# Optimization experiments

Hardware: AMD Instinct MI355X
Metric: run time of the kernel (lower is better)

The kernel has to match this reference:

```python
import jax, jax.numpy as jnp
import numpy as np

NPOINT, RADIUS, NSAMPLE = 1024, 0.4, 32
BN_EPS = 1e-5


def fps(xyz, npoint):
    # xyz: [B, N, 3]. Deterministic start at index 0 (torch uses randint).
    B, N, _ = xyz.shape

    def step(carry, _):
        distance, farthest = carry  # [B,N], [B]
        centroid = jnp.take_along_axis(xyz, farthest[:, None, None], axis=1)  # [B,1,3]
        dist = jnp.sum((xyz - centroid) ** 2, -1)  # [B,N]
        distance = jnp.minimum(distance, dist)
        new_far = jnp.argmax(distance, axis=-1).astype(jnp.int32)
        return (distance, new_far), farthest

    init = (jnp.full((B, N), 1e10, xyz.dtype), jnp.zeros((B,), jnp.int32))
    _, cents = jax.lax.scan(step, init, None, length=npoint)  # [npoint, B]
    return cents.T  # [B, npoint]


def square_distance(src, dst):
    # src [B,S,3], dst [B,N,3] -> [B,S,N]
    d = -2.0 * jnp.einsum('bsc,bnc->bsn', src, dst)
    d = d + jnp.sum(src ** 2, -1)[:, :, None] + jnp.sum(dst ** 2, -1)[:, None, :]
    return jnp.clip(d, 1e-12, None)


def query_ball_point(radius, nsample, xyz, new_xyz):
    B, N, _ = xyz.shape
    S = new_xyz.shape[1]
    sqr = square_distance(new_xyz, xyz)  # [B,S,N]
    gi = jnp.where(sqr > radius ** 2, N, jnp.arange(N, dtype=jnp.int32)[None, None, :])
    gi = jnp.sort(gi, axis=-1)[:, :, :nsample]  # [B,S,K]
    first = gi[:, :, :1]
    return jnp.where(gi == N, first, gi)


def gather_points(points, idx):
    # points [B,N,C], idx [B,S,K] -> [B,S,K,C]
    B, S, K = idx.shape
    C = points.shape[-1]
    flat = jnp.take_along_axis(points, idx.reshape(B, S * K)[:, :, None], axis=1)
    return flat.reshape(B, S, K, C)


def setup_inputs() -> dict:
    key = jax.random.key(0)
    ks = jax.random.split(key, 10)
    B, N, D = 8, 4096, 64
    inp = {
        'xyz': jax.random.normal(ks[0], (B, 3, N), jnp.float32),
        'points': jax.random.normal(ks[1], (B, D, N), jnp.float32),
    }
    chans = [67, 64, 64, 128]
    for i in range(3):
        cin, cout = chans[i], chans[i + 1]
        inp[f'W{i}'] = jax.random.normal(ks[2 + i], (cout, cin), jnp.float32) * (1.0 / np.sqrt(cin))
        inp[f'b{i}'] = jnp.zeros((cout,), jnp.float32)
        inp[f'g{i}'] = jnp.ones((cout,), jnp.float32)
        inp[f'bt{i}'] = jnp.zeros((cout,), jnp.float32)
    return inp


def _forward(xyz, points, Ws, bs, gs, bts):
    xyz_t = jnp.transpose(xyz, (0, 2, 1))      # [B,N,3]
    pts_t = jnp.transpose(points, (0, 2, 1))   # [B,N,D]
    B, N, _ = xyz_t.shape

    fps_idx = fps(xyz_t, NPOINT)                              # [B,S]
    new_xyz = jnp.take_along_axis(xyz_t, fps_idx[:, :, None], axis=1)  # [B,S,3]
    idx = query_ball_point(RADIUS, NSAMPLE, xyz_t, new_xyz)   # [B,S,K]

    grouped_xyz = gather_points(xyz_t, idx)                   # [B,S,K,3]
    grouped_xyz_norm = grouped_xyz - new_xyz[:, :, None, :]
    grouped_pts = gather_points(pts_t, idx)                   # [B,S,K,D]
    new_points = jnp.concatenate([grouped_xyz_norm, grouped_pts], -1)  # [B,S,K,3+D]

    x = jnp.transpose(new_points, (0, 3, 2, 1))  # [B,C,K,S]
    for W, b, g, bt in zip(Ws, bs, gs, bts):
        x = jnp.einsum('oc,bcks->boks', W, x) + b[None, :, None, None]
        mean = jnp.mean(x, axis=(0, 2, 3), keepdims=True)
        var = jnp.var(x, axis=(0, 2, 3), keepdims=True)
        x = (x - mean) * jax.lax.rsqrt(var + BN_EPS)
        x = x * g[None, :, None, None] + bt[None, :, None, None]
        x = jax.nn.relu(x)
    out = jnp.max(x, axis=2)                      # [B,C_out,S]
    return jnp.transpose(new_xyz, (0, 2, 1)), out


def reference(xyz, points, W0, b0, g0, bt0, W1, b1, g1, bt1, W2, b2, g2, bt2):
    return _forward(xyz, points, (W0, W1, W2), (b0, b1, b2), (g0, g1, g2), (bt0, bt1, bt2))
```

## Files before the change

### kernel.cpp

```cpp
#include <hip/hip_runtime.h>
#include <cstddef>
#include <cstdint>

#define NB 8
#define NPTS 4096
#define NS 1024
#define NK 32
#define ND 64

typedef __attribute__((ext_vector_type(8))) short bf16x8;
typedef __attribute__((ext_vector_type(4))) float f32x4;

__device__ __forceinline__ short f2bf(float f) {
  unsigned u = __float_as_uint(f);
  u += 0x7FFF + ((u >> 16) & 1);
  return (short)(u >> 16);
}

#define DPP_IMAX(v, ctrl)                                                     \
  {                                                                           \
    int _o = __builtin_amdgcn_update_dpp(v, v, ctrl, 0xf, 0xf, false);        \
    v = (_o > v) ? _o : v;                                                    \
  }

#define DPP_U64MAX(hi, lo, ctrl)                                              \
  {                                                                           \
    unsigned _nh = (unsigned)__builtin_amdgcn_update_dpp((int)(hi), (int)(hi),\
                                                         ctrl, 0xf, 0xf, false);\
    unsigned _nl = (unsigned)__builtin_amdgcn_update_dpp((int)(lo), (int)(lo),\
                                                         ctrl, 0xf, 0xf, false);\
    bool _gt = (_nh > (hi)) || (_nh == (hi) && _nl > (lo));                   \
    hi = _gt ? _nh : (hi);                                                    \
    lo = _gt ? _nl : (lo);                                                    \
  }

#define DPP_FADD(v, ctrl)                                                     \
  {                                                                           \
    int _t = __builtin_amdgcn_update_dpp(__float_as_int(v), __float_as_int(v),\
                                         ctrl, 0xf, 0xf, false);              \
    v = v + __int_as_float(_t);                                               \
  }

#define DPP_RED16(v, OP)                                                      \
  {                                                                           \
    int _i;                                                                   \
    _i = __builtin_amdgcn_update_dpp(__float_as_int(v), __float_as_int(v), 0x111, 0xf, 0xf, false); \
    v = OP(v, __int_as_float(_i));                                            \
    _i = __builtin_amdgcn_update_dpp(__float_as_int(v), __float_as_int(v), 0x112, 0xf, 0xf, false); \
    v = OP(v, __int_as_float(_i));                                            \
    _i = __builtin_amdgcn_update_dpp(__float_as_int(v), __float_as_int(v), 0x114, 0xf, 0xf, false); \
    v = OP(v, __int_as_float(_i));                                            \
    _i = __builtin_amdgcn_update_dpp(__float_as_int(v), __float_as_int(v), 0x118, 0xf, 0xf, false); \
    v = OP(v, __int_as_float(_i));                                            \
  }

__device__ __forceinline__ float fadd_op(float a, float b) { return a + b; }

__global__ __launch_bounds__(512) void fps_pgemm_kernel(
    const float* __restrict__ xyz, float* __restrict__ out_newxyz,
    float* __restrict__ ws_newxyz, const float* __restrict__ points,
    const float* __restrict__ W0, const float* __restrict__ b0g,
    float* __restrict__ P1) {
  __shared__ __align__(16) char smem[53376];
  const int t = threadIdx.x;

  if (blockIdx.x < 8) {
    float* sXYZ = (float*)smem;
    unsigned long long(*sRed)[8] =
        (unsigned long long(*)[8])(smem + 49152);
    int* sWidx = (int*)(smem + 49280);
    const int b = blockIdx.x;
    const int wave = t >> 6;
    const int lane = t & 63;
    const float* xb = xyz + (size_t)b * 3 * NPTS;

    for (int i = t; i < NPTS; i += 512) {
      sXYZ[i * 3 + 0] = xb[i];
      sXYZ[i * 3 + 1] = xb[NPTS + i];
      sXYZ[i * 3 + 2] = xb[2 * NPTS + i];
    }
    if (t == 0) sWidx[0] = 0;

    float px[8], py[8], pz[8], dist[8];
    {
      float4 a0 = ((const float4*)xb)[2 * t];
      float4 a1 = ((const float4*)xb)[2 * t + 1];
      float4 b0v = ((const float4*)(xb + NPTS))[2 * t];
      float4 b1v = ((const float4*)(xb + NPTS))[2 * t + 1];
      float4 c0 = ((const float4*)(xb + 2 * NPTS))[2 * t];
      float4 c1 = ((const float4*)(xb + 2 * NPTS))[2 * t + 1];
      px[0] = a0.x; px[1] = a0.y; px[2] = a0.z; px[3] = a0.w;
      px[4] = a1.x; px[5] = a1.y; px[6] = a1.z; px[7] = a1.w;
      py[0] = b0v.x; py[1] = b0v.y; py[2] = b0v.z; py[3] = b0v.w;
      py[4] = b1v.x; py[5] = b1v.y; py[6] = b1v.z; py[7] = b1v.w;
      pz[0] = c0.x; pz[1] = c0.y; pz[2] = c0.z; pz[3] = c0.w;
      pz[4] = c1.x; pz[5] = c1.y; pz[6] = c1.z; pz[7] = c1.w;
    }
#pragma unroll
    for (int j = 0; j < 8; ++j) dist[j] = 1e10f;

    float cx = xb[0], cy = xb[NPTS], cz = xb[2 * NPTS];

    for (int s = 0; s < NS; ++s) {
#pragma unroll
      for (int j = 0; j < 8; ++j) {
        float dx = __fadd_rn(px[j], -cx);
        float dy = __fadd_rn(py[j], -cy);
        float dz = __fadd_rn(pz[j], -cz);
        float d = __fadd_rn(__fadd_rn(__fmul_rn(dx, dx), __fmul_rn(dy, dy)),
                            __fmul_rn(dz, dz));
        dist[j] = fminf(dist[j], d);
      }
      float m = fmaxf(fmaxf(fmaxf(dist[0], dist[1]), fmaxf(dist[2], dist[3])),
                      fmaxf(fmaxf(dist[4], dist[5]), fmaxf(dist[6], dist[7])));
      int v = __float_as_int(m);
      DPP_IMAX(v, 0x111)
      DPP_IMAX(v, 0x112)
      DPP_IMAX(v, 0x114)
      DPP_IMAX(v, 0x118)
      DPP_IMAX(v, 0x142)
      DPP_IMAX(v, 0x143)
      const int wm_i = __builtin_amdgcn_readlane(v, 63);
      const float wm = __int_as_float(wm_i);
      unsigned long long claim = __ballot(m == wm);
      int firstlane = __ffsll(claim) - 1;
      if (lane == firstlane) {
        int j = 7;
#pragma unroll
        for (int jj = 6; jj >= 0; --jj)
          if (dist[jj] == wm) j = jj;
        unsigned widx = (unsigned)(t * 8 + j);
        sRed[s & 1][wave] = ((unsigned long long)(unsigned)wm_i << 32) |
                            (unsigned long long)(0xFFFFFFFFu - widx);
      }
      __syncthreads();
      unsigned long long k = sRed[s & 1][lane & 7];
      unsigned h2 = (unsigned)(k >> 32), l2 = (unsigned)k;
      DPP_U64MAX(h2, l2, 0x111)
      DPP_U64MAX(h2, l2, 0x112)
      DPP_U64MAX(h2, l2, 0x114)
      const unsigned gl = (unsigned)__builtin_amdgcn_readlane((int)l2, 7);
      const int widx = (int)(0xFFFFFFFFu - gl);
      cx = sXYZ[widx * 3 + 0];
      cy = sXYZ[widx * 3 + 1];
      cz = sXYZ[widx * 3 + 2];
      if (t == 0 && s < NS - 1) sWidx[s + 1] = widx;
    }
    __syncthreads();
    for (int s2 = t; s2 < NS; s2 += 512) {
      int w = sWidx[s2];
      float x = sXYZ[w * 3 + 0], y = sXYZ[w * 3 + 1], z = sXYZ[w * 3 + 2];
      out_newxyz[b * 3 * NS + s2] = x;
      out_newxyz[b * 3 * NS + NS + s2] = y;
      out_newxyz[b * 3 * NS + 2 * NS + s2] = z;
      ws_newxyz[((b << 10) + s2) * 3 + 0] = x;
      ws_newxyz[((b << 10) + s2) * 3 + 1] = y;
      ws_newxyz[((b << 10) + s2) * 3 + 2] = z;
    }
  } else {
    float* sP = (float*)smem;
    float* sW = (float*)(smem + 16384);
    float* sB = (float*)(smem + 33792);
    const int blk = blockIdx.x - 8;
    const int bb = blk >> 6;
    const int n0 = (blk & 63) * 64;
    const float* pb = points + (size_t)bb * ND * NPTS;
    for (int f = t; f < 4096; f += 512) {
      int c = f >> 6, n = f & 63;
      sP[f] = pb[c * NPTS + n0 + n];
    }
    for (int f = t; f < 4096; f += 512) {
      int c = f >> 6, o = f & 63;
      sW[c * 68 + o] = W0[o * 67 + 3 + c];
    }
    if (t < 64) sB[t] = b0g[t];
    __syncthreads();
    if (t < 256) {
      const int nl = (t & 15) * 4;
      const int ol = (t >> 4) * 4;
      float acc[4][4];
#pragma unroll
      for (int i = 0; i < 4; ++i)
#pragma unroll
        for (int j = 0; j < 4; ++j) acc[i][j] = 0.f;
#pragma unroll 4
      for (int c = 0; c < 64; ++c) {
        float4 xv = *(const float4*)(sP + c * 64 + nl);
        float4 wv = *(const float4*)(sW + c * 68 + ol);
        float xa[4] = {xv.x, xv.y, xv.z, xv.w};
        float wa[4] = {wv.x, wv.y, wv.z, wv.w};
#pragma unroll
        for (int i = 0; i < 4; ++i)
#pragma unroll
          for (int j = 0; j < 4; ++j) acc[i][j] += xa[i] * wa[j];
      }
#pragma unroll
      for (int i = 0; i < 4; ++i) {
        float4 v = make_float4(acc[i][0] + sB[ol + 0], acc[i][1] + sB[ol + 1],
                               acc[i][2] + sB[ol + 2], acc[i][3] + sB[ol + 3]);
        *(float4*)(P1 + ((size_t)(bb << 12) + n0 + nl + i) * 64 + ol) = v;
      }
    }
  }
}

__global__ __launch_bounds__(256) void query_gstats_kernel(
    const float* __restrict__ xyz, const float* __restrict__ ws_newxyz,
    const float* __restrict__ P1, const float* __restrict__ W0,
    int* __restrict__ idx_ws, float* __restrict__ partials) {
  const int w = threadIdx.x >> 6;
  const int lane = threadIdx.x & 63;
  const int p = blockIdx.x * 4 + w;
  const int b = p >> 10;
  __shared__ int sIdx[4][32];
  __shared__ float sWS[4][64];
  __shared__ float sWQ[4][64];
  const float* xb = xyz + (size_t)b * 3 * NPTS;
  const float cx = ws_newxyz[p * 3 + 0];
  const float cy = ws_newxyz[p * 3 + 1];
  const float cz = ws_newxyz[p * 3 + 2];
  const float ss = __fadd_rn(__fadd_rn(__fmul_rn(cx, cx), __fmul_rn(cy, cy)), __fmul_rn(cz, cz));
  const float r2 = (float)(0.4 * 0.4);
  int cnt = 0;
  for (int ci = 0; ci < 64 && cnt < 32; ++ci) {
    int n = ci * 64 + lane;
    float x = xb[n], y = xb[NPTS + n], z = xb[2 * NPTS + n];
    float dot = __fadd_rn(__fadd_rn(__fmul_rn(cx, x), __fmul_rn(cy, y)), __fmul_rn(cz, z));
    float dd = __fadd_rn(__fadd_rn(__fmul_rn(x, x), __fmul_rn(y, y)), __fmul_rn(z, z));
    float d = __fmul_rn(-2.0f, dot);
    d = __fadd_rn(d, ss);
    d = __fadd_rn(d, dd);
    d = fmaxf(d, 1e-12f);
    bool inc = (d <= r2);
    unsigned long long m = __ballot(inc);
    int slot = cnt + (int)__popcll(m & ((1ull << lane) - 1ull));
    if (inc && slot < 32) sIdx[w][slot] = n;
    cnt += (int)__popcll(m);
  }
  if (lane < 32) {
    int v;
    if (lane < cnt) v = sIdx[w][lane];
    else v = (cnt > 0) ? sIdx[w][0] : 0;
    idx_ws[p * 32 + lane] = v;
    sIdx[w][lane] = v;
  }
  const float wx = W0[lane * 67 + 0];
  const float wy = W0[lane * 67 + 1];
  const float wz = W0[lane * 67 + 2];
  float ssum = 0.f, ssq = 0.f;
  for (int r = 0; r < 32; ++r) {
    const int n = sIdx[w][r];
    float P1v = P1[((size_t)(b << 12) + n) * 64 + lane];
    float dx = __fadd_rn(xb[n], -cx);
    float dy = __fadd_rn(xb[NPTS + n], -cy);
    float dz = __fadd_rn(xb[2 * NPTS + n], -cz);
    float y = P1v + (dx * wx + dy * wy + dz * wz);
    ssum += y;
    ssq += y * y;
  }
  sWS[w][lane] = ssum;
  sWQ[w][lane] = ssq;
  __syncthreads();
  const int t = threadIdx.x;
  if (t < 64) {
    float s1 = sWS[0][t] + sWS[1][t] + sWS[2][t] + sWS[3][t];
    float s2 = sWQ[0][t] + sWQ[1][t] + sWQ[2][t] + sWQ[3][t];
    partials[(size_t)blockIdx.x * 128 + t] = s1;
    partials[(size_t)blockIdx.x * 128 + 64 + t] = s2;
  }
}

__global__ __launch_bounds__(256) void conv1_mfma_kernel(
    const float* __restrict__ xyz, const float* __restrict__ P1,
    const int* __restrict__ idx_ws, const float* __restrict__ cen_ws,
    const float* __restrict__ W0, const float* __restrict__ W1,
    const float* __restrict__ b1, const float* __restrict__ scaleA,
    const float* __restrict__ shiftA, float* __restrict__ y1,
    float* __restrict__ partials) {
  __shared__ __align__(16) short sW1b[64 * 72];
  __shared__ __align__(16) short sXb[64 * 72];
  __shared__ int sIdx[64];
  __shared__ float sCen[2 * 4];
  __shared__ float sBias[64], sSum[64], sSq[64];

  const int t = threadIdx.x;
  const int wv = t >> 6, lane = t & 63;
  const int quad = lane >> 4, l15 = lane & 15;
  const int pair0 = blockIdx.x * 2;
  const int b = pair0 >> 10;

  for (int f = t; f < 4096; f += 256) sW1b[(f >> 6) * 72 + (f & 63)] = f2bf(W1[f]);
  if (t < 64) { sBias[t] = b1[t]; sIdx[t] = idx_ws[pair0 * 32 + t]; }
  if (t < 6) sCen[(t / 3) * 4 + (t % 3)] = cen_ws[pair0 * 3 + t];
  const float wx = W0[lane * 67 + 0];
  const float wy = W0[lane * 67 + 1];
  const float wz = W0[lane * 67 + 2];
  const float sc = scaleA[lane];
  const float sh = shiftA[lane];
  __syncthreads();
  const float* xb = xyz + (size_t)b * 3 * NPTS;
  for (int r = wv; r < 64; r += 4) {
    const int sl = r >> 5;
    const int n = sIdx[r];
    float P1v = P1[((size_t)(b << 12) + n) * 64 + lane];
    float dx = __fadd_rn(xb[n], -sCen[sl * 4 + 0]);
    float dy = __fadd_rn(xb[NPTS + n], -sCen[sl * 4 + 1]);
    float dz = __fadd_rn(xb[2 * NPTS + n], -sCen[sl * 4 + 2]);
    float y0 = P1v + (dx * wx + dy * wy + dz * wz);
    sXb[r * 72 + lane] = f2bf(fmaxf(y0 * sc + sh, 0.f));
  }
  __syncthreads();

  f32x4 acc[4];
#pragma unroll
  for (int i = 0; i < 4; ++i) acc[i] = (f32x4){0.f, 0.f, 0.f, 0.f};
#pragma unroll
  for (int kh = 0; kh < 2; ++kh) {
    const int kc = kh * 32 + quad * 8;
    bf16x8 A = *(const bf16x8*)(sW1b + (wv * 16 + l15) * 72 + kc);
#pragma unroll
    for (int ti = 0; ti < 4; ++ti) {
      bf16x8 B = *(const bf16x8*)(sXb + (ti * 16 + l15) * 72 + kc);
      acc[ti] = __builtin_amdgcn_mfma_f32_16x16x32_bf16(A, B, acc[ti], 0, 0, 0);
    }
  }

#pragma unroll
  for (int reg = 0; reg < 4; ++reg) {
    const int m = wv * 16 + quad * 4 + reg;
    const float bb = sBias[m];
    float v[4];
#pragma unroll
    for (int ti = 0; ti < 4; ++ti) {
      v[ti] = acc[ti][reg] + bb;
      y1[(size_t)(pair0 + (ti >> 1)) * 2048 + m * 32 + (ti & 1) * 16 + l15] = v[ti];
    }
    float s1 = (v[0] + v[1]) + (v[2] + v[3]);
    float s2 = (v[0] * v[0] + v[1] * v[1]) + (v[2] * v[2] + v[3] * v[3]);
    DPP_RED16(s1, fadd_op)
    DPP_RED16(s2, fadd_op)
    if (l15 == 15) { sSum[m] = s1; sSq[m] = s2; }
  }
  __syncthreads();
  if (t < 64) {
    partials[(size_t)blockIdx.x * 128 + t] = sSum[t];
    partials[(size_t)blockIdx.x * 128 + 64 + t] = sSq[t];
  }
}

__global__ __launch_bounds__(256) void conv2_mfma_kernel(
    const float* __restrict__ y1, const float* __restrict__ W2,
    const float* __restrict__ b2, const float* __restrict__ scaleA,
    const float* __restrict__ shiftA, float* __restrict__ pmax,
    float* __restrict__ pmin, float* __restrict__ partials) {
  __shared__ __align__(16) short sW2[128 * 72];
  __shared__ __align__(16) short sXb[64 * 72];
  __shared__ float sScale[64], sShift[64], sBias[128];
  __shared__ float sSum[128], sSq[128];
  __shared__ float sMax[2][128], sMin[2][128];

  const int t = threadIdx.x;
  const int pair0 = blockIdx.x * 2;
  const int lane = t & 63;
  const int wv = t >> 6;
  const int quad = lane >> 4;
  const int l15 = lane & 15;

  if (t < 64) { sScale[t] = scaleA[t]; sShift[t] = shiftA[t]; }
  if (t < 128) sBias[t] = b2[t];
  for (int f = t; f < 8192; f += 256) {
    int o = f >> 6, c = f & 63;
    sW2[o * 72 + c] = f2bf(W2[f]);
  }
  for (int f = t; f < 4096; f += 256) {
    int si = f >> 11;
    int rmd = f & 2047;
    int o = rmd >> 5, k = rmd & 31;
    float v = y1[(size_t)(pair0 + si) * 2048 + rmd];
    v = v * sScale[o] + sShift[o];
    v = fmaxf(v, 0.f);
    sXb[(si * 32 + k) * 72 + o] = f2bf(v);
  }
  __syncthreads();

  f32x4 acc[2][4];
#pragma unroll
  for (int i = 0; i < 2; ++i)
#pragma unroll
    for (int ti = 0; ti < 4; ++ti) acc[i][ti] = (f32x4){0.f, 0.f, 0.f, 0.f};
#pragma unroll
  for (int kh = 0; kh < 2; ++kh) {
    const int kc = kh * 32 + quad * 8;
    bf16x8 A0 = *(const bf16x8*)(sW2 + (wv * 32 + l15) * 72 + kc);
    bf16x8 A1 = *(const bf16x8*)(sW2 + (wv * 32 + 16 + l15) * 72 + kc);
#pragma unroll
    for (int ti = 0; ti < 4; ++ti) {
      bf16x8 B = *(const bf16x8*)(sXb + (ti * 16 + l15) * 72 + kc);
      acc[0][ti] = __builtin_amdgcn_mfma_f32_16x16x32_bf16(A0, B, acc[0][ti], 0, 0, 0);
      acc[1][ti] = __builtin_amdgcn_mfma_f32_16x16x32_bf16(A1, B, acc[1][ti], 0, 0, 0);
    }
  }

#pragma unroll
  for (int i = 0; i < 2; ++i) {
#pragma unroll
    for (int reg = 0; reg < 4; ++reg) {
      const int m = wv * 32 + i * 16 + quad * 4 + reg;
      const float bb = sBias[m];
      float v0 = acc[i][0][reg] + bb;
      float v1 = acc[i][1][reg] + bb;
      float v2 = acc[i][2][reg] + bb;
      float v3 = acc[i][3][reg] + bb;
      float s1 = (v0 + v1) + (v2 + v3);
      float s2 = (v0 * v0 + v1 * v1) + (v2 * v2 + v3 * v3);
      float mx0 = fmaxf(v0, v1), mn0 = fminf(v0, v1);
      float mx1 = fmaxf(v2, v3), mn1 = fminf(v2, v3);
      DPP_RED16(s1, fadd_op)
      DPP_RED16(s2, fadd_op)
      DPP_RED16(mx0, fmaxf)
      DPP_RED16(mn0, fminf)
      DPP_RED16(mx1, fmaxf)
      DPP_RED16(mn1, fminf)
      if (l15 == 15) {
        sSum[m] = s1;
        sSq[m] = s2;
        sMax[0][m] = mx0;
        sMin[0][m] = mn0;
        sMax[1][m] = mx1;
        sMin[1][m] = mn1;
      }
    }
  }
  __syncthreads();
  if (t < 128) {
    partials[(size_t)blockIdx.x * 256 + t] = sSum[t];
    partials[(size_t)blockIdx.x * 256 + 128 + t] = sSq[t];
    pmax[(size_t)pair0 * 128 + t] = sMax[0][t];
    pmin[(size_t)pair0 * 128 + t] = sMin[0][t];
    pmax[(size_t)(pair0 + 1) * 128 + t] = sMax[1][t];
    pmin[(size_t)(pair0 + 1) * 128 + t] = sMin[1][t];
  }
}

template <int COUT>
__global__ __launch_bounds__(256) void stats_kernel(const float* __restrict__ partials,
                                                    int nblocks,
                                                    const float* __restrict__ gA,
                                                    const float* __restrict__ btA,
                                                    float* __restrict__ scaleA,
                                                    float* __restrict__ shiftA) {
  const int o = blockIdx.x;
  const int t = threadIdx.x;
  double s1 = 0.0, s2 = 0.0;
  for (int blk = t; blk < nblocks; blk += 256) {
    s1 += (double)partials[(size_t)blk * (COUT * 2) + o];
    s2 += (double)partials[(size_t)blk * (COUT * 2) + COUT + o];
  }
  __shared__ double r1[256], r2[256];
  r1[t] = s1; r2[t] = s2;
  __syncthreads();
  for (int st = 128; st > 0; st >>= 1) {
    if (t < st) { r1[t] += r1[t + st]; r2[t] += r2[t + st]; }
    __syncthreads();
  }
  if (t == 0) {
    const double Nr = 262144.0;
    double mean = r1[0] / Nr;
    double var = r2[0] / Nr - mean * mean;
    double rstd = 1.0 / sqrt(var + 1e-5);
    double sc = rstd * (double)gA[o];
    scaleA[o] = (float)sc;
    shiftA[o] = (float)((double)btA[o] - mean * sc);
  }
}

__global__ __launch_bounds__(256) void stats_final_kernel(
    const float* __restrict__ partials, int nblocks,
    const float* __restrict__ pmax, const float* __restrict__ pmin,
    const float* __restrict__ gA, const float* __restrict__ btA,
    float* __restrict__ out) {
  const int o = blockIdx.x;
  const int t = threadIdx.x;
  double s1 = 0.0, s2 = 0.0;
  for (int blk = t; blk < nblocks; blk += 256) {
    s1 += (double)partials[(size_t)blk * 256 + o];
    s2 += (double)partials[(size_t)blk * 256 + 128 + o];
  }
  __shared__ double r1[256], r2[256];
  __shared__ float sMean, sRstd;
  r1[t] = s1; r2[t] = s2;
  __syncthreads();
  for (int st = 128; st > 0; st >>= 1) {
    if (t < st) { r1[t] += r1[t + st]; r2[t] += r2[t + st]; }
    __syncthreads();
  }
  if (t == 0) {
    const double Nr = 262144.0;
    double mean = r1[0] / Nr;
    double var = r2[0] / Nr - mean * mean;
    sMean = (float)mean;
    sRstd = (float)(1.0 / sqrt(var + 1e-5));
  }
  __syncthreads();
  const float mn = sMean, rs = sRstd, gg = gA[o], bb = btA[o];
  const float slope = rs * gg;
  const float* src = (slope >= 0.f) ? pmax : pmin;
  for (int i = t; i < NB * NS; i += 256) {
    int b = i >> 10;
    int s = i & 1023;
    float v = src[(size_t)i * 128 + o];
    float t1 = (v - mn) * rs;
    float t2 = t1 * gg + bb;
    out[(size_t)b * (128 * NS) + o * NS + s] = fmaxf(t2, 0.f);
  }
}

extern "C" void kernel_launch(void* const* d_in, const int* in_sizes, int n_in,
                              void* d_out, int out_size, void* d_ws, size_t ws_size,
                              hipStream_t stream) {
  (void)in_sizes; (void)n_in; (void)out_size; (void)ws_size;
  const float* xyz = (const float*)d_in[0];
  const float* points = (const float*)d_in[1];
  const float* W0 = (const float*)d_in[2];
  const float* b0 = (const float*)d_in[3];
  const float* g0 = (const float*)d_in[4];
  const float* bt0 = (const float*)d_in[5];
  const float* W1 = (const float*)d_in[6];
  const float* b1 = (const float*)d_in[7];
  const float* g1 = (const float*)d_in[8];
  const float* bt1 = (const float*)d_in[9];
  const float* W2 = (const float*)d_in[10];
  const float* b2 = (const float*)d_in[11];
  const float* g2 = (const float*)d_in[12];
  const float* bt2 = (const float*)d_in[13];
  float* out = (float*)d_out;

  float* ws = (float*)d_ws;
  size_t off = 0;
  float* newxyz = ws + off;  off += (size_t)NB * NS * 3;
  int* idx = (int*)(ws + off); off += (size_t)NB * NS * NK;
  float* P1 = ws + off;      off += (size_t)NB * NPTS * 64;
  float* y1 = ws + off;      off += (size_t)NB * NS * 64 * 32;
  float* partials = ws + off; off += (size_t)8192 * 256;
  float* scaleA = ws + off;  off += 128;
  float* shiftA = ws + off;  off += 128;
  float* pmaxb = ws + off;   off += (size_t)NB * NS * 128;
  float* pminb = ws + off;   off += (size_t)NB * NS * 128;

  fps_pgemm_kernel<<<520, 512, 0, stream>>>(xyz, out, newxyz, points, W0, b0, P1);
  query_gstats_kernel<<<2048, 256, 0, stream>>>(xyz, newxyz, P1, W0, idx, partials);
  stats_kernel<64><<<64, 256, 0, stream>>>(partials, 2048, g0, bt0, scaleA, shiftA);
  conv1_mfma_kernel<<<4096, 256, 0, stream>>>(xyz, P1, idx, newxyz, W0, W1, b1,
                                              scaleA, shiftA, y1, partials);
  stats_kernel<64><<<64, 256, 0, stream>>>(partials, 4096, g1, bt1, scaleA, shiftA);
  conv2_mfma_kernel<<<4096, 256, 0, stream>>>(y1, W2, b2, scaleA, shiftA,
                                              pmaxb, pminb, partials);
  stats_final_kernel<<<128, 256, 0, stream>>>(partials, 4096, pmaxb, pminb,
                                              g2, bt2, out + NB * NS * 3);
}
```

Before: 969.2 us.

## Process four centroids per block in conv kernels and transpose max/min buffers

conv1 and conv2 now handle four centroid groups per block instead of two. The number of blocks halves, and each block loads and converts its weight tile to bf16 over twice as much work. Per-block statistics and per-centroid max/min are written to global memory straight from the DPP reduction lanes, which removes the shared-memory staging and the final barrier. The max/min buffers are stored channel-major, so the final kernel reads them contiguously. In exchange each block uses more registers and LDS, which may lower occupancy, and there are fewer blocks to spread across the GPU.

```diff
diff --git a/kernel.cpp b/kernel.cpp
--- a/kernel.cpp
+++ b/kernel.cpp
@@ -32,13 +32,6 @@
     bool _gt = (_nh > (hi)) || (_nh == (hi) && _nl > (lo));                   \
     hi = _gt ? _nh : (hi);                                                    \
     lo = _gt ? _nl : (lo);                                                    \
-  }
-
-#define DPP_FADD(v, ctrl)                                                     \
-  {                                                                           \
-    int _t = __builtin_amdgcn_update_dpp(__float_as_int(v), __float_as_int(v),\
-                                         ctrl, 0xf, 0xf, false);              \
-    v = v + __int_as_float(_t);                                               \
   }
 
 #define DPP_RED16(v, OP)                                                      \
@@ -278,20 +271,21 @@
     const float* __restrict__ shiftA, float* __restrict__ y1,
     float* __restrict__ partials) {
   __shared__ __align__(16) short sW1b[64 * 72];
-  __shared__ __align__(16) short sXb[64 * 72];
-  __shared__ int sIdx[64];
-  __shared__ float sCen[2 * 4];
-  __shared__ float sBias[64], sSum[64], sSq[64];
+  __shared__ __align__(16) short sXb[128 * 72];
+  __shared__ int sIdx[128];
+  __shared__ float sCen[4 * 4];
+  __shared__ float sBias[64];
 
   const int t = threadIdx.x;
   const int wv = t >> 6, lane = t & 63;
   const int quad = lane >> 4, l15 = lane & 15;
-  const int pair0 = blockIdx.x * 2;
+  const int pair0 = blockIdx.x * 4;
   const int b = pair0 >> 10;
 
   for (int f = t; f < 4096; f += 256) sW1b[(f >> 6) * 72 + (f & 63)] = f2bf(W1[f]);
-  if (t < 64) { sBias[t] = b1[t]; sIdx[t] = idx_ws[pair0 * 32 + t]; }
-  if (t < 6) sCen[(t / 3) * 4 + (t % 3)] = cen_ws[pair0 * 3 + t];
+  if (t < 64) sBias[t] = b1[t];
+  if (t < 128) sIdx[t] = idx_ws[pair0 * 32 + t];
+  if (t < 12) sCen[(t / 3) * 4 + (t % 3)] = cen_ws[pair0 * 3 + t];
   const float wx = W0[lane * 67 + 0];
   const float wy = W0[lane * 67 + 1];
   const float wz = W0[lane * 67 + 2];
@@ -299,7 +293,7 @@
   const float sh = shiftA[lane];
   __syncthreads();
   const float* xb = xyz + (size_t)b * 3 * NPTS;
-  for (int r = wv; r < 64; r += 4) {
+  for (int r = wv; r < 128; r += 4) {
     const int sl = r >> 5;
     const int n = sIdx[r];
     float P1v = P1[((size_t)(b << 12) + n) * 64 + lane];
@@ -311,15 +305,15 @@
   }
   __syncthreads();
 
-  f32x4 acc[4];
-#pragma unroll
-  for (int i = 0; i < 4; ++i) acc[i] = (f32x4){0.f, 0.f, 0.f, 0.f};
+  f32x4 acc[8];
+#pragma unroll
+  for (int i = 0; i < 8; ++i) acc[i] = (f32x4){0.f, 0.f, 0.f, 0.f};
 #pragma unroll
   for (int kh = 0; kh < 2; ++kh) {
     const int kc = kh * 32 + quad * 8;
     bf16x8 A = *(const bf16x8*)(sW1b + (wv * 16 + l15) * 72 + kc);
 #pragma unroll
-    for (int ti = 0; ti < 4; ++ti) {
+    for (int ti = 0; ti < 8; ++ti) {
       bf16x8 B = *(const bf16x8*)(sXb + (ti * 16 + l15) * 72 + kc);
       acc[ti] = __builtin_amdgcn_mfma_f32_16x16x32_bf16(A, B, acc[ti], 0, 0, 0);
     }
@@ -329,38 +323,35 @@
   for (int reg = 0; reg < 4; ++reg) {
     const int m = wv * 16 + quad * 4 + reg;
     const float bb = sBias[m];
-    float v[4];
-#pragma unroll
-    for (int ti = 0; ti < 4; ++ti) {
+    float v[8];
+#pragma unroll
+    for (int ti = 0; ti < 8; ++ti) {
       v[ti] = acc[ti][reg] + bb;
       y1[(size_t)(pair0 + (ti >> 1)) * 2048 + m * 32 + (ti & 1) * 16 + l15] = v[ti];
     }
-    float s1 = (v[0] + v[1]) + (v[2] + v[3]);
-    float s2 = (v[0] * v[0] + v[1] * v[1]) + (v[2] * v[2] + v[3] * v[3]);
+    float s1 = ((v[0] + v[1]) + (v[2] + v[3])) + ((v[4] + v[5]) + (v[6] + v[7]));
+    float s2 = ((v[0] * v[0] + v[1] * v[1]) + (v[2] * v[2] + v[3] * v[3])) +
+               ((v[4] * v[4] + v[5] * v[5]) + (v[6] * v[6] + v[7] * v[7]));
     DPP_RED16(s1, fadd_op)
     DPP_RED16(s2, fadd_op)
-    if (l15 == 15) { sSum[m] = s1; sSq[m] = s2; }
-  }
-  __syncthreads();
-  if (t < 64) {
-    partials[(size_t)blockIdx.x * 128 + t] = sSum[t];
-    partials[(size_t)blockIdx.x * 128 + 64 + t] = sSq[t];
+    if (l15 == 15) {
+      partials[(size_t)blockIdx.x * 128 + m] = s1;
+      partials[(size_t)blockIdx.x * 128 + 64 + m] = s2;
+    }
   }
 }
 
 __global__ __launch_bounds__(256) void conv2_mfma_kernel(
     const float* __restrict__ y1, const float* __restrict__ W2,
     const float* __restrict__ b2, const float* __restrict__ scaleA,
-    const float* __restrict__ shiftA, float* __restrict__ pmax,
-    float* __restrict__ pmin, float* __restrict__ partials) {
+    const float* __restrict__ shiftA, float* __restrict__ pmaxT,
+    float* __restrict__ pminT, float* __restrict__ partials) {
   __shared__ __align__(16) short sW2[128 * 72];
-  __shared__ __align__(16) short sXb[64 * 72];
+  __shared__ __align__(16) short sXb[128 * 72];
   __shared__ float sScale[64], sShift[64], sBias[128];
-  __shared__ float sSum[128], sSq[128];
-  __shared__ float sMax[2][128], sMin[2][128];
 
   const int t = threadIdx.x;
-  const int pair0 = blockIdx.x * 2;
+  const int pair0 = blockIdx.x * 4;
   const int lane = t & 63;
   const int wv = t >> 6;
   const int quad = lane >> 4;
@@ -372,7 +363,7 @@
     int o = f >> 6, c = f & 63;
     sW2[o * 72 + c] = f2bf(W2[f]);
   }
-  for (int f = t; f < 4096; f += 256) {
+  for (int f = t; f < 8192; f += 256) {
     int si = f >> 11;
     int rmd = f & 2047;
     int o = rmd >> 5, k = rmd & 31;
@@ -383,18 +374,18 @@
   }
   __syncthreads();
 
-  f32x4 acc[2][4];
+  f32x4 acc[2][8];
 #pragma unroll
   for (int i = 0; i < 2; ++i)
 #pragma unroll
-    for (int ti = 0; ti < 4; ++ti) acc[i][ti] = (f32x4){0.f, 0.f, 0.f, 0.f};
+    for (int ti = 0; ti < 8; ++ti) acc[i][ti] = (f32x4){0.f, 0.f, 0.f, 0.f};
 #pragma unroll
   for (int kh = 0; kh < 2; ++kh) {
     const int kc = kh * 32 + quad * 8;
     bf16x8 A0 = *(const bf16x8*)(sW2 + (wv * 32 + l15) * 72 + kc);
     bf16x8 A1 = *(const bf16x8*)(sW2 + (wv * 32 + 16 + l15) * 72 + kc);
 #pragma unroll
-    for (int ti = 0; ti < 4; ++ti) {
+    for (int ti = 0; ti < 8; ++ti) {
       bf16x8 B = *(const bf16x8*)(sXb + (ti * 16 + l15) * 72 + kc);
       acc[0][ti] = __builtin_amdgcn_mfma_f32_16x16x32_bf16(A0, B, acc[0][ti], 0, 0, 0);
       acc[1][ti] = __builtin_amdgcn_mfma_f32_16x16x32_bf16(A1, B, acc[1][ti], 0, 0, 0);
@@ -407,38 +398,30 @@
     for (int reg = 0; reg < 4; ++reg) {
       const int m = wv * 32 + i * 16 + quad * 4 + reg;
       const float bb = sBias[m];
-      float v0 = acc[i][0][reg] + bb;
-      float v1 = acc[i][1][reg] + bb;
-      float v2 = acc[i][2][reg] + bb;
-      float v3 = acc[i][3][reg] + bb;
-      float s1 = (v0 + v1) + (v2 + v3);
-      float s2 = (v0 * v0 + v1 * v1) + (v2 * v2 + v3 * v3);
-      float mx0 = fmaxf(v0, v1), mn0 = fminf(v0, v1);
-      float mx1 = fmaxf(v2, v3), mn1 = fminf(v2, v3);
+      float v[8];
+#pragma unroll
+      for (int ti = 0; ti < 8; ++ti) v[ti] = acc[i][ti][reg] + bb;
+      float s1 = ((v[0] + v[1]) + (v[2] + v[3])) + ((v[4] + v[5]) + (v[6] + v[7]));
+      float s2 = ((v[0] * v[0] + v[1] * v[1]) + (v[2] * v[2] + v[3] * v[3])) +
+                 ((v[4] * v[4] + v[5] * v[5]) + (v[6] * v[6] + v[7] * v[7]));
       DPP_RED16(s1, fadd_op)
       DPP_RED16(s2, fadd_op)
-      DPP_RED16(mx0, fmaxf)
-      DPP_RED16(mn0, fminf)
-      DPP_RED16(mx1, fmaxf)
-      DPP_RED16(mn1, fminf)
       if (l15 == 15) {
-        sSum[m] = s1;
-        sSq[m] = s2;
-        sMax[0][m] = mx0;
-        sMin[0][m] = mn0;
-        sMax[1][m] = mx1;
-        sMin[1][m] = mn1;
+        partials[(size_t)blockIdx.x * 256 + m] = s1;
+        partials[(size_t)blockIdx.x * 256 + 128 + m] = s2;
       }
-    }
-  }
-  __syncthreads();
-  if (t < 128) {
-    partials[(size_t)blockIdx.x * 256 + t] = sSum[t];
-    partials[(size_t)blockIdx.x * 256 + 128 + t] = sSq[t];
-    pmax[(size_t)pair0 * 128 + t] = sMax[0][t];
-    pmin[(size_t)pair0 * 128 + t] = sMin[0][t];
-    pmax[(size_t)(pair0 + 1) * 128 + t] = sMax[1][t];
-    pmin[(size_t)(pair0 + 1) * 128 + t] = sMin[1][t];
+#pragma unroll
+      for (int si = 0; si < 4; ++si) {
+        float mx = fmaxf(v[2 * si], v[2 * si + 1]);
+        float mn = fminf(v[2 * si], v[2 * si + 1]);
+        DPP_RED16(mx, fmaxf)
+        DPP_RED16(mn, fminf)
+        if (l15 == 15) {
+          pmaxT[(size_t)m * 8192 + pair0 + si] = mx;
+          pminT[(size_t)m * 8192 + pair0 + si] = mn;
+        }
+      }
+    }
   }
 }
 
@@ -476,7 +459,7 @@
 
 __global__ __launch_bounds__(256) void stats_final_kernel(
     const float* __restrict__ partials, int nblocks,
-    const float* __restrict__ pmax, const float* __restrict__ pmin,
+    const float* __restrict__ pmaxT, const float* __restrict__ pminT,
     const float* __restrict__ gA, const float* __restrict__ btA,
     float* __restrict__ out) {
   const int o = blockIdx.x;
@@ -504,11 +487,11 @@
   __syncthreads();
   const float mn = sMean, rs = sRstd, gg = gA[o], bb = btA[o];
   const float slope = rs * gg;
-  const float* src = (slope >= 0.f) ? pmax : pmin;
+  const float* src = (slope >= 0.f) ? pmaxT : pminT;
   for (int i = t; i < NB * NS; i += 256) {
     int b = i >> 10;
     int s = i & 1023;
-    float v = src[(size_t)i * 128 + o];
+    float v = src[(size_t)o * 8192 + i];
     float t1 = (v - mn) * rs;
     float t2 = t1 * gg + bb;
     out[(size_t)b * (128 * NS) + o * NS + s] = fmaxf(t2, 0.f);
@@ -544,17 +527,17 @@
   float* partials = ws + off; off += (size_t)8192 * 256;
   float* scaleA = ws + off;  off += 128;
   float* shiftA = ws + off;  off += 128;
-  float* pmaxb = ws + off;   off += (size_t)NB * NS * 128;
-  float* pminb = ws + off;   off += (size_t)NB * NS * 128;
+  float* pmaxT = ws + off;   off += (size_t)128 * NB * NS;
+  float* pminT = ws + off;   off += (size_t)128 * NB * NS;
 
   fps_pgemm_kernel<<<520, 512, 0, stream>>>(xyz, out, newxyz, points, W0, b0, P1);
   query_gstats_kernel<<<2048, 256, 0, stream>>>(xyz, newxyz, P1, W0, idx, partials);
   stats_kernel<64><<<64, 256, 0, stream>>>(partials, 2048, g0, bt0, scaleA, shiftA);
-  conv1_mfma_kernel<<<4096, 256, 0, stream>>>(xyz, P1, idx, newxyz, W0, W1, b1,
+  conv1_mfma_kernel<<<2048, 256, 0, stream>>>(xyz, P1, idx, newxyz, W0, W1, b1,
                                               scaleA, shiftA, y1, partials);
-  stats_kernel<64><<<64, 256, 0, stream>>>(partials, 4096, g1, bt1, scaleA, shiftA);
-  conv2_mfma_kernel<<<4096, 256, 0, stream>>>(y1, W2, b2, scaleA, shiftA,
-                                              pmaxb, pminb, partials);
-  stats_final_kernel<<<128, 256, 0, stream>>>(partials, 4096, pmaxb, pminb,
+  stats_kernel<64><<<64, 256, 0, stream>>>(partials, 2048, g1, bt1, scaleA, shiftA);
+  conv2_mfma_kernel<<<2048, 256, 0, stream>>>(y1, W2, b2, scaleA, shiftA,
+                                              pmaxT, pminT, partials);
+  stats_final_kernel<<<128, 256, 0, stream>>>(partials, 2048, pmaxT, pminT,
                                               g2, bt2, out + NB * NS * 3);
 }
```

New measurement: 951.2 us. About the same (-1.9%).
